# Performance work log

Measured on AMD Instinct MI355X. Metric: run time of the kernel, lower is better.

## Reference

```python
import jax, jax.numpy as jnp
import numpy as np

C = 512
NH = 8
GROUPS = 32
EPS = 1e-5


def setup_inputs() -> dict:
    key = jax.random.key(0)
    ks = jax.random.split(key, 7)
    B, T, H, W = 4, 24, 32, 32
    x = jax.random.normal(ks[0], (B, C, T, H, W), dtype=jnp.float32)
    gn_w = jnp.ones((C,), jnp.float32)
    gn_b = jnp.zeros((C,), jnp.float32)
    # 1x1 Conv1d weights stored as [out_ch, in_ch] (kernel dim of size 1 dropped)
    qkv_w = jax.random.normal(ks[1], (3 * C, C), dtype=jnp.float32) / np.sqrt(C)
    qkv_b = jax.random.normal(ks[2], (3 * C,), dtype=jnp.float32) * 0.02
    proj_w = jax.random.normal(ks[3], (C, C), dtype=jnp.float32) / np.sqrt(C)
    proj_b = jax.random.normal(ks[4], (C,), dtype=jnp.float32) * 0.02
    return {"x": x, "gn_w": gn_w, "gn_b": gn_b, "qkv_w": qkv_w,
            "qkv_b": qkv_b, "proj_w": proj_w, "proj_b": proj_b}


def reference(x, gn_w, gn_b, qkv_w, qkv_b, proj_w, proj_b):
    B, Cc, T, H, W = x.shape
    hd = Cc // NH
    # [B,C,T,H,W] -> [B*H*W, C, T]
    xf = jnp.transpose(x, (0, 3, 4, 1, 2)).reshape(B * H * W, Cc, T)
    # GroupNorm over (C/G, T) per group
    xg = xf.reshape(-1, GROUPS, Cc // GROUPS, T)
    mean = xg.mean(axis=(2, 3), keepdims=True)
    var = xg.var(axis=(2, 3), keepdims=True)
    xn = ((xg - mean) * jax.lax.rsqrt(var + EPS)).reshape(-1, Cc, T)
    xn = xn * gn_w[:, None] + gn_b[:, None]
    # 1x1 conv QKV: [n, 3C, T]
    qkv = jnp.einsum('nct,dc->ndt', xn, qkv_w) + qkv_b[:, None]
    qkv = qkv.reshape(-1, 3, NH, hd, T)
    q, k, v = qkv[:, 0], qkv[:, 1], qkv[:, 2]  # each [n, h, d, T]
    scale = 1.0 / np.sqrt(hd)
    attn = jax.nn.softmax(jnp.einsum('nhdt,nhds->nhts', q, k) * scale, axis=-1)
    out = jnp.einsum('nhts,nhds->nhtd', attn, v)        # [n, h, T, d]
    out = out.transpose(0, 2, 1, 3).reshape(-1, T, Cc)   # [n, T, C]
    out = out.transpose(0, 2, 1)                         # [n, C, T]
    out = jnp.einsum('nct,dc->ndt', out, proj_w) + proj_b[:, None]
    out = out.reshape(B, H, W, Cc, T).transpose(0, 3, 4, 1, 2)
    return x + out
```

## Files before the change

kernel.cpp:

```cpp
#include <hip/hip_runtime.h>
#include <hip/hip_bf16.h>
#include <stdint.h>

#define C_    512
#define T_    24
#define HWSZ  1024
#define NN    4096
#define JTOT  98304
#define EPSV  1e-5f

typedef short short8 __attribute__((ext_vector_type(8)));
typedef short short4v __attribute__((ext_vector_type(4)));
typedef float f32x4 __attribute__((ext_vector_type(4)));

typedef __attribute__((address_space(1))) const uint32_t glob_u32;
typedef __attribute__((address_space(3))) uint32_t lds_u32;

__device__ __forceinline__ unsigned short f2bf(float f) {
  union { float f; unsigned u; } v; v.f = f;
  unsigned r = v.u + 0x7fffu + ((v.u >> 16) & 1u);
  return (unsigned short)(r >> 16);
}
__device__ __forceinline__ float bf2f(unsigned short b) {
  union { unsigned u; float f; } v; v.u = ((unsigned)b) << 16;
  return v.f;
}
__device__ __forceinline__ float bflo(uint32_t u) {
  union { unsigned u; float f; } v; v.u = u << 16; return v.f;
}
__device__ __forceinline__ float bfhi(uint32_t u) {
  union { unsigned u; float f; } v; v.u = u & 0xffff0000u; return v.f;
}
__device__ __forceinline__ uint32_t pkbf(float a, float b) {
  return (uint32_t)f2bf(a) | ((uint32_t)f2bf(b) << 16);
}

__device__ __forceinline__ void gload_lds16(const void* g, void* l) {
  __builtin_amdgcn_global_load_lds((glob_u32*)g, (lds_u32*)l, 16, 0, 0);
}

__global__ void k_cvt(const float* __restrict__ qkvw, const float* __restrict__ projw,
                      unsigned short* __restrict__ qkvw_bf, unsigned short* __restrict__ projw_bf) {
  int i = blockIdx.x * 256 + threadIdx.x;
  if (i < 786432) qkvw_bf[i] = f2bf(qkvw[i]);
  if (i < 262144) projw_bf[i] = f2bf(projw[i]);
}

__global__ __launch_bounds__(256) void k_stats(const float* __restrict__ x,
                                               float* __restrict__ mean, float* __restrict__ rstd) {
  int bid = blockIdx.x;
  int g = bid & 31, hwt = (bid >> 5) & 15, b = bid >> 9;
  int tid = threadIdx.x, lane = tid & 63, grp = tid >> 6;
  int hw = hwt * 64 + lane;
  float s = 0.f, sq = 0.f;
  for (int ct = grp; ct < 384; ct += 4) {
    int c = g * 16 + ct / 24;
    int t = ct % 24;
    float v = x[((size_t)((b * 512 + c) * 24 + t) << 10) + hw];
    s += v; sq += v * v;
  }
  __shared__ float ls[4][64], lq[4][64];
  ls[grp][lane] = s; lq[grp][lane] = sq;
  __syncthreads();
  if (tid < 64) {
    float S = ls[0][tid] + ls[1][tid] + ls[2][tid] + ls[3][tid];
    float Q = lq[0][tid] + lq[1][tid] + lq[2][tid] + lq[3][tid];
    float m = S * (1.f / 384.f);
    float var = Q * (1.f / 384.f) - m * m;
    int n = b * HWSZ + hwt * 64 + tid;
    mean[n * 32 + g] = m;
    rstd[n * 32 + g] = rsqrtf(var + EPSV);
  }
}

__global__ __launch_bounds__(256) void k_norm(const float* __restrict__ x,
                                              const float* __restrict__ mean, const float* __restrict__ rstd,
                                              const float* __restrict__ gnw, const float* __restrict__ gnb,
                                              unsigned short* __restrict__ xn) {
  __shared__ unsigned short xs[64][260];
  const int bid = blockIdx.x;
  const int hwt = bid & 15;
  const int chalf = (bid >> 4) & 1;
  const int tb = bid >> 5;
  const int t = tb % 24, b = tb / 24;
  const int hw0 = hwt * 64;
  const int tid = threadIdx.x;
  const int w = tid >> 6, lane = tid & 63;

  const int crel0 = w * 4 + (lane >> 4);
  const int hwr = (lane & 15) * 4;
#pragma unroll
  for (int k = 0; k < 16; ++k) {
    const int crel = k * 16 + crel0;
    const int c = chalf * 256 + crel;
    const float4 v = *reinterpret_cast<const float4*>(
        &x[(((size_t)(b * 512 + c) * 24 + t) << 10) + hw0 + hwr]);
    xs[hwr + 0][crel] = f2bf(v.x);
    xs[hwr + 1][crel] = f2bf(v.y);
    xs[hwr + 2][crel] = f2bf(v.z);
    xs[hwr + 3][crel] = f2bf(v.w);
  }

  const int crel8 = (lane & 31) * 8;
  const int c8 = chalf * 256 + crel8;
  const int g = c8 >> 4;
  float gw[8], gb[8];
#pragma unroll
  for (int i = 0; i < 8; ++i) { gw[i] = gnw[c8 + i]; gb[i] = gnb[c8 + i]; }
  float mm[8], rr[8];
#pragma unroll
  for (int p = 0; p < 8; ++p) {
    const int nrel = (p * 4 + w) * 2 + (lane >> 5);
    const int ng = b * HWSZ + hw0 + nrel;
    mm[p] = mean[ng * 32 + g];
    rr[p] = rstd[ng * 32 + g];
  }
  __syncthreads();

#pragma unroll
  for (int p = 0; p < 8; ++p) {
    const int nrel = (p * 4 + w) * 2 + (lane >> 5);
    const short4v lo = *reinterpret_cast<const short4v*>(&xs[nrel][crel8]);
    const short4v hi = *reinterpret_cast<const short4v*>(&xs[nrel][crel8 + 4]);
    float y[8];
#pragma unroll
    for (int i = 0; i < 4; ++i) {
      y[i]     = (bf2f((unsigned short)lo[i]) - mm[p]) * rr[p] * gw[i]     + gb[i];
      y[i + 4] = (bf2f((unsigned short)hi[i]) - mm[p]) * rr[p] * gw[i + 4] + gb[i + 4];
    }
    uint4 wv;
    wv.x = pkbf(y[0], y[1]);
    wv.y = pkbf(y[2], y[3]);
    wv.z = pkbf(y[4], y[5]);
    wv.w = pkbf(y[6], y[7]);
    const size_t j = (size_t)t * NN + b * HWSZ + hw0 + nrel;
    *reinterpret_cast<uint4*>(&xn[j * C_ + c8]) = wv;
  }
}

#define STAGE8(mat, half, tile, Gptr, row0)                                           \
  {                                                                                   \
    unsigned short* _l = &lds[(((tile) & 1) * 2 + (mat))][half][(w * 2) * 512];       \
    const unsigned short* _g = (Gptr) +                                               \
        (size_t)((row0) + (half) * 128 + (w * 2) * 8 + srow) * 512 +                  \
        (tile) * 64 + sslot * 8;                                                      \
    gload_lds16(_g, _l);                                                              \
    gload_lds16(_g + 8 * 512, _l + 512);                                              \
  }

__global__ __launch_bounds__(512, 2) void k_gemm8(
    const unsigned short* __restrict__ A,
    const unsigned short* __restrict__ B,
    const float* __restrict__ bias,
    unsigned short* __restrict__ outb) {
  __shared__ __attribute__((aligned(16))) unsigned short lds[4][2][8192];
  const int bid = blockIdx.x;
  const int cpx = 2304 >> 3;
  const int lid = (bid & 7) * cpx + (bid >> 3);
  const int mt = lid % 6, jt = lid / 6;
  const int m0 = mt * 256, j0 = jt * 256;
  const int tid = threadIdx.x;
  const int w = tid >> 6, lane = tid & 63;
  const int l16 = lane & 15, lqq = lane >> 4;
  const int wm = w >> 2, wn = w & 3;
  const int srow = lane >> 3;
  const int sslot = (lane & 7) ^ srow;
  const int k0off = l16 * 64 + ((lqq ^ (l16 & 7)) * 8);
  const int k1off = l16 * 64 + (((lqq + 4) ^ (l16 & 7)) * 8);

  f32x4 acc[8][4];
#pragma unroll
  for (int i = 0; i < 8; ++i)
#pragma unroll
    for (int j = 0; j < 4; ++j) acc[i][j] = {0.f, 0.f, 0.f, 0.f};

  STAGE8(0, 0, 0, A, m0); STAGE8(0, 1, 0, A, m0);
  STAGE8(1, 0, 0, B, j0); STAGE8(1, 1, 0, B, j0);
  STAGE8(0, 0, 1, A, m0); STAGE8(0, 1, 1, A, m0);
  STAGE8(1, 0, 1, B, j0);
  asm volatile("s_waitcnt vmcnt(6)" ::: "memory");
  __builtin_amdgcn_s_barrier();

  for (int t = 0; t < 8; ++t) {
    const int buf = t & 1;
    const unsigned short* Ab = &lds[buf * 2 + 0][wm][0];
    const unsigned short* Bb = &lds[buf * 2 + 1][wn >> 1][(wn & 1) * 4096];
    short8 a[8][2], bb[4][2];
#pragma unroll
    for (int rr = 0; rr < 8; ++rr) {
      a[rr][0] = *reinterpret_cast<const short8*>(Ab + rr * 1024 + k0off);
      a[rr][1] = *reinterpret_cast<const short8*>(Ab + rr * 1024 + k1off);
    }
#pragma unroll
    for (int cc = 0; cc < 2; ++cc) {
      bb[cc][0] = *reinterpret_cast<const short8*>(Bb + cc * 1024 + k0off);
      bb[cc][1] = *reinterpret_cast<const short8*>(Bb + cc * 1024 + k1off);
    }
    if (t < 7) STAGE8(1, 1, t + 1, B, j0);
    asm volatile("" ::: "memory");
    __builtin_amdgcn_s_barrier();
    asm volatile("s_waitcnt lgkmcnt(0)" ::: "memory");
    __builtin_amdgcn_sched_barrier(0);
    __builtin_amdgcn_s_setprio(1);
#pragma unroll
    for (int rr = 0; rr < 4; ++rr)
#pragma unroll
      for (int cc = 0; cc < 2; ++cc) {
        acc[rr][cc] = __builtin_amdgcn_mfma_f32_16x16x32_bf16(a[rr][0], bb[cc][0], acc[rr][cc], 0, 0, 0);
        acc[rr][cc] = __builtin_amdgcn_mfma_f32_16x16x32_bf16(a[rr][1], bb[cc][1], acc[rr][cc], 0, 0, 0);
      }
    __builtin_amdgcn_s_setprio(0);
    asm volatile("" ::: "memory");
    __builtin_amdgcn_s_barrier();
#pragma unroll
    for (int cc = 2; cc < 4; ++cc) {
      bb[cc][0] = *reinterpret_cast<const short8*>(Bb + cc * 1024 + k0off);
      bb[cc][1] = *reinterpret_cast<const short8*>(Bb + cc * 1024 + k1off);
    }
    if (t < 6) STAGE8(0, 0, t + 2, A, m0);
    asm volatile("" ::: "memory");
    __builtin_amdgcn_s_barrier();
    asm volatile("s_waitcnt lgkmcnt(0)" ::: "memory");
    __builtin_amdgcn_sched_barrier(0);
    __builtin_amdgcn_s_setprio(1);
#pragma unroll
    for (int rr = 0; rr < 4; ++rr)
#pragma unroll
      for (int cc = 2; cc < 4; ++cc) {
        acc[rr][cc] = __builtin_amdgcn_mfma_f32_16x16x32_bf16(a[rr][0], bb[cc][0], acc[rr][cc], 0, 0, 0);
        acc[rr][cc] = __builtin_amdgcn_mfma_f32_16x16x32_bf16(a[rr][1], bb[cc][1], acc[rr][cc], 0, 0, 0);
      }
    __builtin_amdgcn_s_setprio(0);
    asm volatile("" ::: "memory");
    __builtin_amdgcn_s_barrier();
    if (t < 6) STAGE8(0, 1, t + 2, A, m0);
    asm volatile("" ::: "memory");
    __builtin_amdgcn_s_barrier();
    __builtin_amdgcn_s_setprio(1);
#pragma unroll
    for (int rr = 4; rr < 8; ++rr)
#pragma unroll
      for (int cc = 0; cc < 2; ++cc) {
        acc[rr][cc] = __builtin_amdgcn_mfma_f32_16x16x32_bf16(a[rr][0], bb[cc][0], acc[rr][cc], 0, 0, 0);
        acc[rr][cc] = __builtin_amdgcn_mfma_f32_16x16x32_bf16(a[rr][1], bb[cc][1], acc[rr][cc], 0, 0, 0);
      }
    __builtin_amdgcn_s_setprio(0);
    asm volatile("" ::: "memory");
    __builtin_amdgcn_s_barrier();
    if (t < 6) STAGE8(1, 0, t + 2, B, j0);
    asm volatile("" ::: "memory");
    __builtin_amdgcn_s_barrier();
    __builtin_amdgcn_s_setprio(1);
#pragma unroll
    for (int rr = 4; rr < 8; ++rr)
#pragma unroll
      for (int cc = 2; cc < 4; ++cc) {
        acc[rr][cc] = __builtin_amdgcn_mfma_f32_16x16x32_bf16(a[rr][0], bb[cc][0], acc[rr][cc], 0, 0, 0);
        acc[rr][cc] = __builtin_amdgcn_mfma_f32_16x16x32_bf16(a[rr][1], bb[cc][1], acc[rr][cc], 0, 0, 0);
      }
    __builtin_amdgcn_s_setprio(0);
    asm volatile("" ::: "memory");
    if (t < 6) {
      asm volatile("s_waitcnt vmcnt(6)" ::: "memory");
    } else if (t == 6) {
      asm volatile("s_waitcnt vmcnt(0)" ::: "memory");
    }
    __builtin_amdgcn_s_barrier();
  }

#pragma unroll
  for (int rr = 0; rr < 8; ++rr) {
#pragma unroll
    for (int cc = 0; cc < 4; ++cc) {
      const int row = m0 + wm * 128 + rr * 16 + lqq * 4;
      const int col = j0 + wn * 64 + cc * 16 + l16;
#pragma unroll
      for (int r = 0; r < 4; ++r) {
        float v = acc[rr][cc][r] + bias[row + r];
        outb[(size_t)(row + r) * JTOT + col] = f2bf(v);
      }
    }
  }
}

template <int MODE>
__global__ __launch_bounds__(256, 3) void k_gemm(
    const unsigned short* __restrict__ A,
    const unsigned short* __restrict__ B,
    const float* __restrict__ bias,
    unsigned short* __restrict__ outb,
    const float* __restrict__ xres,
    float* __restrict__ outf) {
  __shared__ __attribute__((aligned(16))) unsigned short As[128 * 64];
  __shared__ __attribute__((aligned(16))) unsigned short Bs[128 * 64];
  const int NMT = (MODE == 0) ? 12 : 4;
  const int bid = blockIdx.x;
  const int cpx = gridDim.x >> 3;
  const int lid = (bid & 7) * cpx + (bid >> 3);
  const int mt = lid % NMT, jt = lid / NMT;
  const int j0 = jt * 128, m0 = mt * 128;
  const int tid = threadIdx.x;
  const int wave = tid >> 6, lane = tid & 63;
  const int l16 = lane & 15, lqq = lane >> 4;
  const int wm = wave >> 1, wn = wave & 1;
  const int srow = lane >> 3, sseg = lane & 7;

  f32x4 acc[4][4];
#pragma unroll
  for (int i = 0; i < 4; ++i)
#pragma unroll
    for (int j = 0; j < 4; ++j) acc[i][j] = {0.f, 0.f, 0.f, 0.f};

  for (int kt = 0; kt < 512; kt += 64) {
#pragma unroll
    for (int i = 0; i < 4; ++i) {
      const int chunk = i * 4 + wave;
      const int r = chunk * 8 + srow;
      gload_lds16(A + ((size_t)(m0 + r) * 512 + kt + sseg * 8), &As[chunk * 512]);
    }
    if (MODE == 0) {
#pragma unroll
      for (int i = 0; i < 4; ++i) {
        const int chunk = i * 4 + wave;
        const int r = chunk * 8 + srow;
        gload_lds16(B + ((size_t)(j0 + r) * 512 + kt + sseg * 8), &Bs[chunk * 512]);
      }
    } else {
#pragma unroll
      for (int p = 0; p < 4; ++p) {
        const int u = p * 256 + tid;
        const int kc = u >> 7, jr = u & 127;
        gload_lds16(B + ((size_t)((kt >> 3) + kc) * JTOT + (j0 + jr)) * 8, &Bs[(size_t)u * 8]);
      }
    }
    __syncthreads();
#pragma unroll
    for (int ks = 0; ks < 2; ++ks) {
      short8 af[4], bfr[4];
#pragma unroll
      for (int i = 0; i < 4; ++i)
        af[i] = *reinterpret_cast<const short8*>(&As[(wm * 64 + i * 16 + l16) * 64 + ks * 32 + lqq * 8]);
#pragma unroll
      for (int i = 0; i < 4; ++i) {
        if (MODE == 0)
          bfr[i] = *reinterpret_cast<const short8*>(&Bs[(wn * 64 + i * 16 + l16) * 64 + ks * 32 + lqq * 8]);
        else
          bfr[i] = *reinterpret_cast<const short8*>(&Bs[(((ks * 4 + lqq) * 128) + wn * 64 + i * 16 + l16) * 8]);
      }
#pragma unroll
      for (int mi = 0; mi < 4; ++mi)
#pragma unroll
        for (int ni = 0; ni < 4; ++ni)
          acc[mi][ni] = __builtin_amdgcn_mfma_f32_16x16x32_bf16(af[mi], bfr[ni], acc[mi][ni], 0, 0, 0);
    }
    __syncthreads();
  }

#pragma unroll
  for (int mi = 0; mi < 4; ++mi) {
#pragma unroll
    for (int ni = 0; ni < 4; ++ni) {
      const int dbase = m0 + wm * 64 + mi * 16 + lqq * 4;
      const int jj = j0 + wn * 64 + ni * 16 + l16;
      if (MODE == 0) {
#pragma unroll
        for (int r = 0; r < 4; ++r) {
          float v = acc[mi][ni][r] + bias[dbase + r];
          outb[(size_t)(dbase + r) * JTOT + jj] = f2bf(v);
        }
      } else {
        const int t = jj >> 12, n = jj & 4095;
        const int b = n >> 10, hw = n & 1023;
#pragma unroll
        for (int r = 0; r < 4; ++r) {
          size_t o = (((size_t)(b * 512 + dbase + r) * 24 + t) << 10) + hw;
          outf[o] = xres[o] + acc[mi][ni][r] + bias[dbase + r];
        }
      }
    }
  }
}

__global__ __launch_bounds__(512) void k_attn(const unsigned short* __restrict__ qkv,
                                              unsigned short* __restrict__ aoC) {
  __shared__ uint32_t kbuf[4][24][64];
  const int ntile = blockIdx.x, h = blockIdx.y;
  const int n0 = ntile * 64;
  const int lane = threadIdx.x & 63, slot = threadIdx.x >> 6;
  const int t0 = slot * 3;
  const size_t baseq = (size_t)(h * 64) * JTOT + n0 + lane;
  const size_t basek = (size_t)(512 + h * 64) * JTOT + n0 + lane;
  const size_t basev = (size_t)(1024 + h * 64) * JTOT + n0 + lane;

  float S[3][24];
#pragma unroll
  for (int a = 0; a < 3; ++a)
#pragma unroll
    for (int s = 0; s < 24; ++s) S[a][s] = 0.f;

  uint32_t kp[12], qp[12];

#pragma unroll
  for (int dp = 0; dp < 4; ++dp)
#pragma unroll
    for (int a = 0; a < 3; ++a) {
      uint32_t klo = qkv[basek + (size_t)(2 * dp) * JTOT + (t0 + a) * NN];
      uint32_t khi = qkv[basek + (size_t)(2 * dp + 1) * JTOT + (t0 + a) * NN];
      kp[dp * 3 + a] = klo | (khi << 16);
      uint32_t qlo = qkv[baseq + (size_t)(2 * dp) * JTOT + (t0 + a) * NN];
      uint32_t qhi = qkv[baseq + (size_t)(2 * dp + 1) * JTOT + (t0 + a) * NN];
      qp[dp * 3 + a] = qlo | (qhi << 16);
    }

  for (int c = 0; c < 8; ++c) {
    const int dc = c * 8;
#pragma unroll
    for (int dp = 0; dp < 4; ++dp)
#pragma unroll
      for (int a = 0; a < 3; ++a)
        kbuf[dp][t0 + a][lane] = kp[dp * 3 + a];
    float qf[3][8];
#pragma unroll
    for (int dp = 0; dp < 4; ++dp)
#pragma unroll
      for (int a = 0; a < 3; ++a) {
        qf[a][2 * dp]     = bflo(qp[dp * 3 + a]);
        qf[a][2 * dp + 1] = bfhi(qp[dp * 3 + a]);
      }
    if (c < 7) {
      const int dn = dc + 8;
#pragma unroll
      for (int dp = 0; dp < 4; ++dp)
#pragma unroll
        for (int a = 0; a < 3; ++a) {
          uint32_t klo = qkv[basek + (size_t)(dn + 2 * dp) * JTOT + (t0 + a) * NN];
          uint32_t khi = qkv[basek + (size_t)(dn + 2 * dp + 1) * JTOT + (t0 + a) * NN];
          kp[dp * 3 + a] = klo | (khi << 16);
          uint32_t qlo = qkv[baseq + (size_t)(dn + 2 * dp) * JTOT + (t0 + a) * NN];
          uint32_t qhi = qkv[baseq + (size_t)(dn + 2 * dp + 1) * JTOT + (t0 + a) * NN];
          qp[dp * 3 + a] = qlo | (qhi << 16);
        }
    }
    __syncthreads();
#pragma unroll
    for (int dp = 0; dp < 4; ++dp) {
#pragma unroll
      for (int s = 0; s < 24; ++s) {
        uint32_t kpr = kbuf[dp][s][lane];
        float k0 = bflo(kpr), k1 = bfhi(kpr);
        S[0][s] = fmaf(qf[0][2 * dp], k0, S[0][s]);
        S[0][s] = fmaf(qf[0][2 * dp + 1], k1, S[0][s]);
        S[1][s] = fmaf(qf[1][2 * dp], k0, S[1][s]);
        S[1][s] = fmaf(qf[1][2 * dp + 1], k1, S[1][s]);
        S[2][s] = fmaf(qf[2][2 * dp], k0, S[2][s]);
        S[2][s] = fmaf(qf[2][2 * dp + 1], k1, S[2][s]);
      }
    }
    __syncthreads();
  }

#pragma unroll
  for (int dp = 0; dp < 4; ++dp)
#pragma unroll
    for (int a = 0; a < 3; ++a) {
      uint32_t vlo = qkv[basev + (size_t)(2 * dp) * JTOT + (t0 + a) * NN];
      uint32_t vhi = qkv[basev + (size_t)(2 * dp + 1) * JTOT + (t0 + a) * NN];
      kp[dp * 3 + a] = vlo | (vhi << 16);
    }

#pragma unroll
  for (int a = 0; a < 3; ++a) {
    float mx = S[a][0];
#pragma unroll
    for (int s = 1; s < 24; ++s) mx = fmaxf(mx, S[a][s]);
    float sum = 0.f;
#pragma unroll
    for (int s = 0; s < 24; ++s) {
      float e = __expf((S[a][s] - mx) * 0.125f);
      S[a][s] = e; sum += e;
    }
    float inv = 1.f / sum;
#pragma unroll
    for (int s = 0; s < 24; ++s) S[a][s] *= inv;
  }

  for (int c = 0; c < 8; ++c) {
    const int dc = c * 8;
#pragma unroll
    for (int dp = 0; dp < 4; ++dp)
#pragma unroll
      for (int a = 0; a < 3; ++a)
        kbuf[dp][t0 + a][lane] = kp[dp * 3 + a];
    if (c < 7) {
      const int dn = dc + 8;
#pragma unroll
      for (int dp = 0; dp < 4; ++dp)
#pragma unroll
        for (int a = 0; a < 3; ++a) {
          uint32_t vlo = qkv[basev + (size_t)(dn + 2 * dp) * JTOT + (t0 + a) * NN];
          uint32_t vhi = qkv[basev + (size_t)(dn + 2 * dp + 1) * JTOT + (t0 + a) * NN];
          kp[dp * 3 + a] = vlo | (vhi << 16);
        }
    }
    __syncthreads();
    float o[3][8];
#pragma unroll
    for (int a = 0; a < 3; ++a)
#pragma unroll
      for (int d = 0; d < 8; ++d) o[a][d] = 0.f;
#pragma unroll
    for (int dp = 0; dp < 4; ++dp) {
#pragma unroll
      for (int s = 0; s < 24; ++s) {
        uint32_t vpr = kbuf[dp][s][lane];
        float v0 = bflo(vpr), v1 = bfhi(vpr);
        o[0][2 * dp]     = fmaf(S[0][s], v0, o[0][2 * dp]);
        o[0][2 * dp + 1] = fmaf(S[0][s], v1, o[0][2 * dp + 1]);
        o[1][2 * dp]     = fmaf(S[1][s], v0, o[1][2 * dp]);
        o[1][2 * dp + 1] = fmaf(S[1][s], v1, o[1][2 * dp + 1]);
        o[2][2 * dp]     = fmaf(S[2][s], v0, o[2][2 * dp]);
        o[2][2 * dp + 1] = fmaf(S[2][s], v1, o[2][2 * dp + 1]);
      }
    }
#pragma unroll
    for (int a = 0; a < 3; ++a) {
      uint4 wv;
      wv.x = pkbf(o[a][0], o[a][1]);
      wv.y = pkbf(o[a][2], o[a][3]);
      wv.z = pkbf(o[a][4], o[a][5]);
      wv.w = pkbf(o[a][6], o[a][7]);
      size_t unit = (size_t)(h * 8 + c) * JTOT + (size_t)(t0 + a) * NN + n0 + lane;
      *reinterpret_cast<uint4*>(&aoC[unit * 8]) = wv;
    }
    __syncthreads();
  }
}

extern "C" void kernel_launch(void* const* d_in, const int* in_sizes, int n_in,
                              void* d_out, int out_size, void* d_ws, size_t ws_size,
                              hipStream_t stream) {
  (void)in_sizes; (void)n_in; (void)out_size; (void)ws_size;
  const float* x     = (const float*)d_in[0];
  const float* gnw   = (const float*)d_in[1];
  const float* gnb   = (const float*)d_in[2];
  const float* qkvw  = (const float*)d_in[3];
  const float* qkvb  = (const float*)d_in[4];
  const float* projw = (const float*)d_in[5];
  const float* projb = (const float*)d_in[6];
  float* out = (float*)d_out;
  char* ws = (char*)d_ws;

  unsigned short* qkvw_bf = (unsigned short*)(ws);
  unsigned short* projw_bf = (unsigned short*)(ws + 1572864);
  float* mean = (float*)(ws + 2097152);
  float* rstd = (float*)(ws + 2621440);
  unsigned short* xn  = (unsigned short*)(ws + 3145728);
  unsigned short* qkv = (unsigned short*)(ws + 3145728 + 100663296);

  k_cvt<<<dim3(3072), dim3(256), 0, stream>>>(qkvw, projw, qkvw_bf, projw_bf);
  k_stats<<<dim3(2048), dim3(256), 0, stream>>>(x, mean, rstd);
  k_norm<<<dim3(3072), dim3(256), 0, stream>>>(x, mean, rstd, gnw, gnb, xn);
  k_gemm8<<<dim3(2304), dim3(512), 0, stream>>>(qkvw_bf, xn, qkvb, qkv);
  k_attn<<<dim3(64, 8), dim3(512), 0, stream>>>(qkv, xn);
  k_gemm<1><<<dim3(3072), dim3(256), 0, stream>>>(projw_bf, xn, projb, nullptr, x, out);
}
```

Measured before the change: 588.6 us.

## Make 256x256 GEMM persistent and reuse it for output projection

The large-tile bf16 GEMM is converted into a persistent kernel with 256 blocks, each looping over several output tiles in an XCD-grouped order instead of launching one block per tile. It is templated so the output projection, previously run by a smaller 128x128 non-pipelined GEMM, now uses the same pipelined 256x256 path. For that path it adds a separate B-staging routine for the k-chunked attention-output layout and fuses the residual add. This aims to cut launch and tail overhead and raise data reuse in the projection GEMM. The cost is fewer resident blocks and a pipeline prologue that restarts for every tile.

```diff
diff --git a/kernel.cpp b/kernel.cpp
--- a/kernel.cpp
+++ b/kernel.cpp
@@ -148,17 +148,31 @@
     gload_lds16(_g + 8 * 512, _l + 512);                                              \
   }
 
+#define STAGE8B1(half, tile)                                                          \
+  {                                                                                   \
+    unsigned short* _l = &lds[(((tile) & 1) * 2 + 1)][half][(w * 2) * 512];           \
+    const unsigned short* _g = B +                                                    \
+        ((size_t)((tile) * 8 + sslot) * JTOT + (j0 + (half) * 128 + w * 16 + srow)) * 8; \
+    gload_lds16(_g, _l);                                                              \
+    gload_lds16(_g + 64, _l + 512);                                                   \
+  }
+
+#define STAGE_B(half, tile) { if (MODE == 0) { STAGE8(1, half, tile, B, j0) } else { STAGE8B1(half, tile) } }
+
+template <int MODE>
 __global__ __launch_bounds__(512, 2) void k_gemm8(
     const unsigned short* __restrict__ A,
     const unsigned short* __restrict__ B,
     const float* __restrict__ bias,
-    unsigned short* __restrict__ outb) {
+    unsigned short* __restrict__ outb,
+    const float* __restrict__ xres,
+    float* __restrict__ outf) {
   __shared__ __attribute__((aligned(16))) unsigned short lds[4][2][8192];
   const int bid = blockIdx.x;
-  const int cpx = 2304 >> 3;
-  const int lid = (bid & 7) * cpx + (bid >> 3);
-  const int mt = lid % 6, jt = lid / 6;
-  const int m0 = mt * 256, j0 = jt * 256;
+  const int xcd = bid & 7, cu = bid >> 3;
+  const int NMT = (MODE == 0) ? 6 : 2;
+  const int TPX = (MODE == 0) ? 288 : 96;
+  const int ITERS = (MODE == 0) ? 9 : 3;
   const int tid = threadIdx.x;
   const int w = tid >> 6, lane = tid & 63;
   const int l16 = lane & 15, lqq = lane >> 4;
@@ -168,213 +182,131 @@
   const int k0off = l16 * 64 + ((lqq ^ (l16 & 7)) * 8);
   const int k1off = l16 * 64 + (((lqq + 4) ^ (l16 & 7)) * 8);
 
-  f32x4 acc[8][4];
-#pragma unroll
-  for (int i = 0; i < 8; ++i)
-#pragma unroll
-    for (int j = 0; j < 4; ++j) acc[i][j] = {0.f, 0.f, 0.f, 0.f};
-
-  STAGE8(0, 0, 0, A, m0); STAGE8(0, 1, 0, A, m0);
-  STAGE8(1, 0, 0, B, j0); STAGE8(1, 1, 0, B, j0);
-  STAGE8(0, 0, 1, A, m0); STAGE8(0, 1, 1, A, m0);
-  STAGE8(1, 0, 1, B, j0);
-  asm volatile("s_waitcnt vmcnt(6)" ::: "memory");
-  __builtin_amdgcn_s_barrier();
-
-  for (int t = 0; t < 8; ++t) {
-    const int buf = t & 1;
-    const unsigned short* Ab = &lds[buf * 2 + 0][wm][0];
-    const unsigned short* Bb = &lds[buf * 2 + 1][wn >> 1][(wn & 1) * 4096];
-    short8 a[8][2], bb[4][2];
+  for (int it = 0; it < ITERS; ++it) {
+    const int lid = xcd * TPX + it * 32 + cu;
+    const int mt = lid % NMT, jt = lid / NMT;
+    const int m0 = mt * 256, j0 = jt * 256;
+
+    f32x4 acc[8][4];
+#pragma unroll
+    for (int i = 0; i < 8; ++i)
+#pragma unroll
+      for (int j = 0; j < 4; ++j) acc[i][j] = {0.f, 0.f, 0.f, 0.f};
+
+    STAGE8(0, 0, 0, A, m0); STAGE8(0, 1, 0, A, m0);
+    STAGE_B(0, 0); STAGE_B(1, 0);
+    STAGE8(0, 0, 1, A, m0); STAGE8(0, 1, 1, A, m0);
+    STAGE_B(0, 1);
+    asm volatile("s_waitcnt vmcnt(6)" ::: "memory");
+    __builtin_amdgcn_s_barrier();
+
+    for (int t = 0; t < 8; ++t) {
+      const int buf = t & 1;
+      const unsigned short* Ab = &lds[buf * 2 + 0][wm][0];
+      const unsigned short* Bb = &lds[buf * 2 + 1][wn >> 1][(wn & 1) * 4096];
+      short8 a[8][2], bb[4][2];
+#pragma unroll
+      for (int rr = 0; rr < 8; ++rr) {
+        a[rr][0] = *reinterpret_cast<const short8*>(Ab + rr * 1024 + k0off);
+        a[rr][1] = *reinterpret_cast<const short8*>(Ab + rr * 1024 + k1off);
+      }
+#pragma unroll
+      for (int cc = 0; cc < 2; ++cc) {
+        bb[cc][0] = *reinterpret_cast<const short8*>(Bb + cc * 1024 + k0off);
+        bb[cc][1] = *reinterpret_cast<const short8*>(Bb + cc * 1024 + k1off);
+      }
+      if (t < 7) STAGE_B(1, t + 1);
+      asm volatile("" ::: "memory");
+      __builtin_amdgcn_s_barrier();
+      asm volatile("s_waitcnt lgkmcnt(0)" ::: "memory");
+      __builtin_amdgcn_sched_barrier(0);
+      __builtin_amdgcn_s_setprio(1);
+#pragma unroll
+      for (int rr = 0; rr < 4; ++rr)
+#pragma unroll
+        for (int cc = 0; cc < 2; ++cc) {
+          acc[rr][cc] = __builtin_amdgcn_mfma_f32_16x16x32_bf16(a[rr][0], bb[cc][0], acc[rr][cc], 0, 0, 0);
+          acc[rr][cc] = __builtin_amdgcn_mfma_f32_16x16x32_bf16(a[rr][1], bb[cc][1], acc[rr][cc], 0, 0, 0);
+        }
+      __builtin_amdgcn_s_setprio(0);
+      asm volatile("" ::: "memory");
+      __builtin_amdgcn_s_barrier();
+#pragma unroll
+      for (int cc = 2; cc < 4; ++cc) {
+        bb[cc][0] = *reinterpret_cast<const short8*>(Bb + cc * 1024 + k0off);
+        bb[cc][1] = *reinterpret_cast<const short8*>(Bb + cc * 1024 + k1off);
+      }
+      if (t < 6) STAGE8(0, 0, t + 2, A, m0);
+      asm volatile("" ::: "memory");
+      __builtin_amdgcn_s_barrier();
+      asm volatile("s_waitcnt lgkmcnt(0)" ::: "memory");
+      __builtin_amdgcn_sched_barrier(0);
+      __builtin_amdgcn_s_setprio(1);
+#pragma unroll
+      for (int rr = 0; rr < 4; ++rr)
+#pragma unroll
+        for (int cc = 2; cc < 4; ++cc) {
+          acc[rr][cc] = __builtin_amdgcn_mfma_f32_16x16x32_bf16(a[rr][0], bb[cc][0], acc[rr][cc], 0, 0, 0);
+          acc[rr][cc] = __builtin_amdgcn_mfma_f32_16x16x32_bf16(a[rr][1], bb[cc][1], acc[rr][cc], 0, 0, 0);
+        }
+      __builtin_amdgcn_s_setprio(0);
+      asm volatile("" ::: "memory");
+      __builtin_amdgcn_s_barrier();
+      if (t < 6) STAGE8(0, 1, t + 2, A, m0);
+      asm volatile("" ::: "memory");
+      __builtin_amdgcn_s_barrier();
+      __builtin_amdgcn_s_setprio(1);
+#pragma unroll
+      for (int rr = 4; rr < 8; ++rr)
+#pragma unroll
+        for (int cc = 0; cc < 2; ++cc) {
+          acc[rr][cc] = __builtin_amdgcn_mfma_f32_16x16x32_bf16(a[rr][0], bb[cc][0], acc[rr][cc], 0, 0, 0);
+          acc[rr][cc] = __builtin_amdgcn_mfma_f32_16x16x32_bf16(a[rr][1], bb[cc][1], acc[rr][cc], 0, 0, 0);
+        }
+      __builtin_amdgcn_s_setprio(0);
+      asm volatile("" ::: "memory");
+      __builtin_amdgcn_s_barrier();
+      if (t < 6) STAGE_B(0, t + 2);
+      asm volatile("" ::: "memory");
+      __builtin_amdgcn_s_barrier();
+      __builtin_amdgcn_s_setprio(1);
+#pragma unroll
+      for (int rr = 4; rr < 8; ++rr)
+#pragma unroll
+        for (int cc = 2; cc < 4; ++cc) {
+          acc[rr][cc] = __builtin_amdgcn_mfma_f32_16x16x32_bf16(a[rr][0], bb[cc][0], acc[rr][cc], 0, 0, 0);
+          acc[rr][cc] = __builtin_amdgcn_mfma_f32_16x16x32_bf16(a[rr][1], bb[cc][1], acc[rr][cc], 0, 0, 0);
+        }
+      __builtin_amdgcn_s_setprio(0);
+      asm volatile("" ::: "memory");
+      if (t < 6) {
+        asm volatile("s_waitcnt vmcnt(6)" ::: "memory");
+      } else if (t == 6) {
+        asm volatile("s_waitcnt vmcnt(0)" ::: "memory");
+      }
+      __builtin_amdgcn_s_barrier();
+    }
+
 #pragma unroll
     for (int rr = 0; rr < 8; ++rr) {
-      a[rr][0] = *reinterpret_cast<const short8*>(Ab + rr * 1024 + k0off);
-      a[rr][1] = *reinterpret_cast<const short8*>(Ab + rr * 1024 + k1off);
-    }
-#pragma unroll
-    for (int cc = 0; cc < 2; ++cc) {
-      bb[cc][0] = *reinterpret_cast<const short8*>(Bb + cc * 1024 + k0off);
-      bb[cc][1] = *reinterpret_cast<const short8*>(Bb + cc * 1024 + k1off);
-    }
-    if (t < 7) STAGE8(1, 1, t + 1, B, j0);
-    asm volatile("" ::: "memory");
-    __builtin_amdgcn_s_barrier();
-    asm volatile("s_waitcnt lgkmcnt(0)" ::: "memory");
-    __builtin_amdgcn_sched_barrier(0);
-    __builtin_amdgcn_s_setprio(1);
-#pragma unroll
-    for (int rr = 0; rr < 4; ++rr)
-#pragma unroll
-      for (int cc = 0; cc < 2; ++cc) {
-        acc[rr][cc] = __builtin_amdgcn_mfma_f32_16x16x32_bf16(a[rr][0], bb[cc][0], acc[rr][cc], 0, 0, 0);
-        acc[rr][cc] = __builtin_amdgcn_mfma_f32_16x16x32_bf16(a[rr][1], bb[cc][1], acc[rr][cc], 0, 0, 0);
-      }
-    __builtin_amdgcn_s_setprio(0);
-    asm volatile("" ::: "memory");
-    __builtin_amdgcn_s_barrier();
-#pragma unroll
-    for (int cc = 2; cc < 4; ++cc) {
-      bb[cc][0] = *reinterpret_cast<const short8*>(Bb + cc * 1024 + k0off);
-      bb[cc][1] = *reinterpret_cast<const short8*>(Bb + cc * 1024 + k1off);
-    }
-    if (t < 6) STAGE8(0, 0, t + 2, A, m0);
-    asm volatile("" ::: "memory");
-    __builtin_amdgcn_s_barrier();
-    asm volatile("s_waitcnt lgkmcnt(0)" ::: "memory");
-    __builtin_amdgcn_sched_barrier(0);
-    __builtin_amdgcn_s_setprio(1);
-#pragma unroll
-    for (int rr = 0; rr < 4; ++rr)
-#pragma unroll
-      for (int cc = 2; cc < 4; ++cc) {
-        acc[rr][cc] = __builtin_amdgcn_mfma_f32_16x16x32_bf16(a[rr][0], bb[cc][0], acc[rr][cc], 0, 0, 0);
-        acc[rr][cc] = __builtin_amdgcn_mfma_f32_16x16x32_bf16(a[rr][1], bb[cc][1], acc[rr][cc], 0, 0, 0);
-      }
-    __builtin_amdgcn_s_setprio(0);
-    asm volatile("" ::: "memory");
-    __builtin_amdgcn_s_barrier();
-    if (t < 6) STAGE8(0, 1, t + 2, A, m0);
-    asm volatile("" ::: "memory");
-    __builtin_amdgcn_s_barrier();
-    __builtin_amdgcn_s_setprio(1);
-#pragma unroll
-    for (int rr = 4; rr < 8; ++rr)
-#pragma unroll
-      for (int cc = 0; cc < 2; ++cc) {
-        acc[rr][cc] = __builtin_amdgcn_mfma_f32_16x16x32_bf16(a[rr][0], bb[cc][0], acc[rr][cc], 0, 0, 0);
-        acc[rr][cc] = __builtin_amdgcn_mfma_f32_16x16x32_bf16(a[rr][1], bb[cc][1], acc[rr][cc], 0, 0, 0);
-      }
-    __builtin_amdgcn_s_setprio(0);
-    asm volatile("" ::: "memory");
-    __builtin_amdgcn_s_barrier();
-    if (t < 6) STAGE8(1, 0, t + 2, B, j0);
-    asm volatile("" ::: "memory");
-    __builtin_amdgcn_s_barrier();
-    __builtin_amdgcn_s_setprio(1);
-#pragma unroll
-    for (int rr = 4; rr < 8; ++rr)
-#pragma unroll
-      for (int cc = 2; cc < 4; ++cc) {
-        acc[rr][cc] = __builtin_amdgcn_mfma_f32_16x16x32_bf16(a[rr][0], bb[cc][0], acc[rr][cc], 0, 0, 0);
-        acc[rr][cc] = __builtin_amdgcn_mfma_f32_16x16x32_bf16(a[rr][1], bb[cc][1], acc[rr][cc], 0, 0, 0);
-      }
-    __builtin_amdgcn_s_setprio(0);
-    asm volatile("" ::: "memory");
-    if (t < 6) {
-      asm volatile("s_waitcnt vmcnt(6)" ::: "memory");
-    } else if (t == 6) {
-      asm volatile("s_waitcnt vmcnt(0)" ::: "memory");
-    }
-    __builtin_amdgcn_s_barrier();
-  }
-
-#pragma unroll
-  for (int rr = 0; rr < 8; ++rr) {
-#pragma unroll
-    for (int cc = 0; cc < 4; ++cc) {
-      const int row = m0 + wm * 128 + rr * 16 + lqq * 4;
-      const int col = j0 + wn * 64 + cc * 16 + l16;
-#pragma unroll
-      for (int r = 0; r < 4; ++r) {
-        float v = acc[rr][cc][r] + bias[row + r];
-        outb[(size_t)(row + r) * JTOT + col] = f2bf(v);
-      }
-    }
-  }
-}
-
-template <int MODE>
-__global__ __launch_bounds__(256, 3) void k_gemm(
-    const unsigned short* __restrict__ A,
-    const unsigned short* __restrict__ B,
-    const float* __restrict__ bias,
-    unsigned short* __restrict__ outb,
-    const float* __restrict__ xres,
-    float* __restrict__ outf) {
-  __shared__ __attribute__((aligned(16))) unsigned short As[128 * 64];
-  __shared__ __attribute__((aligned(16))) unsigned short Bs[128 * 64];
-  const int NMT = (MODE == 0) ? 12 : 4;
-  const int bid = blockIdx.x;
-  const int cpx = gridDim.x >> 3;
-  const int lid = (bid & 7) * cpx + (bid >> 3);
-  const int mt = lid % NMT, jt = lid / NMT;
-  const int j0 = jt * 128, m0 = mt * 128;
-  const int tid = threadIdx.x;
-  const int wave = tid >> 6, lane = tid & 63;
-  const int l16 = lane & 15, lqq = lane >> 4;
-  const int wm = wave >> 1, wn = wave & 1;
-  const int srow = lane >> 3, sseg = lane & 7;
-
-  f32x4 acc[4][4];
-#pragma unroll
-  for (int i = 0; i < 4; ++i)
-#pragma unroll
-    for (int j = 0; j < 4; ++j) acc[i][j] = {0.f, 0.f, 0.f, 0.f};
-
-  for (int kt = 0; kt < 512; kt += 64) {
-#pragma unroll
-    for (int i = 0; i < 4; ++i) {
-      const int chunk = i * 4 + wave;
-      const int r = chunk * 8 + srow;
-      gload_lds16(A + ((size_t)(m0 + r) * 512 + kt + sseg * 8), &As[chunk * 512]);
-    }
-    if (MODE == 0) {
-#pragma unroll
-      for (int i = 0; i < 4; ++i) {
-        const int chunk = i * 4 + wave;
-        const int r = chunk * 8 + srow;
-        gload_lds16(B + ((size_t)(j0 + r) * 512 + kt + sseg * 8), &Bs[chunk * 512]);
-      }
-    } else {
-#pragma unroll
-      for (int p = 0; p < 4; ++p) {
-        const int u = p * 256 + tid;
-        const int kc = u >> 7, jr = u & 127;
-        gload_lds16(B + ((size_t)((kt >> 3) + kc) * JTOT + (j0 + jr)) * 8, &Bs[(size_t)u * 8]);
-      }
-    }
-    __syncthreads();
-#pragma unroll
-    for (int ks = 0; ks < 2; ++ks) {
-      short8 af[4], bfr[4];
-#pragma unroll
-      for (int i = 0; i < 4; ++i)
-        af[i] = *reinterpret_cast<const short8*>(&As[(wm * 64 + i * 16 + l16) * 64 + ks * 32 + lqq * 8]);
-#pragma unroll
-      for (int i = 0; i < 4; ++i) {
-        if (MODE == 0)
-          bfr[i] = *reinterpret_cast<const short8*>(&Bs[(wn * 64 + i * 16 + l16) * 64 + ks * 32 + lqq * 8]);
-        else
-          bfr[i] = *reinterpret_cast<const short8*>(&Bs[(((ks * 4 + lqq) * 128) + wn * 64 + i * 16 + l16) * 8]);
-      }
-#pragma unroll
-      for (int mi = 0; mi < 4; ++mi)
-#pragma unroll
-        for (int ni = 0; ni < 4; ++ni)
-          acc[mi][ni] = __builtin_amdgcn_mfma_f32_16x16x32_bf16(af[mi], bfr[ni], acc[mi][ni], 0, 0, 0);
-    }
-    __syncthreads();
-  }
-
-#pragma unroll
-  for (int mi = 0; mi < 4; ++mi) {
-#pragma unroll
-    for (int ni = 0; ni < 4; ++ni) {
-      const int dbase = m0 + wm * 64 + mi * 16 + lqq * 4;
-      const int jj = j0 + wn * 64 + ni * 16 + l16;
-      if (MODE == 0) {
-#pragma unroll
-        for (int r = 0; r < 4; ++r) {
-          float v = acc[mi][ni][r] + bias[dbase + r];
-          outb[(size_t)(dbase + r) * JTOT + jj] = f2bf(v);
-        }
-      } else {
-        const int t = jj >> 12, n = jj & 4095;
-        const int b = n >> 10, hw = n & 1023;
-#pragma unroll
-        for (int r = 0; r < 4; ++r) {
-          size_t o = (((size_t)(b * 512 + dbase + r) * 24 + t) << 10) + hw;
-          outf[o] = xres[o] + acc[mi][ni][r] + bias[dbase + r];
+#pragma unroll
+      for (int cc = 0; cc < 4; ++cc) {
+        const int row = m0 + wm * 128 + rr * 16 + lqq * 4;
+        const int col = j0 + wn * 64 + cc * 16 + l16;
+        if (MODE == 0) {
+#pragma unroll
+          for (int r = 0; r < 4; ++r) {
+            float v = acc[rr][cc][r] + bias[row + r];
+            outb[(size_t)(row + r) * JTOT + col] = f2bf(v);
+          }
+        } else {
+          const int t_ = col >> 12, n = col & 4095;
+          const int b_ = n >> 10, hw = n & 1023;
+#pragma unroll
+          for (int r = 0; r < 4; ++r) {
+            size_t o = (((size_t)(b_ * 512 + row + r) * 24 + t_) << 10) + hw;
+            outf[o] = xres[o] + acc[rr][cc][r] + bias[row + r];
+          }
         }
       }
     }
@@ -560,7 +492,7 @@
   k_cvt<<<dim3(3072), dim3(256), 0, stream>>>(qkvw, projw, qkvw_bf, projw_bf);
   k_stats<<<dim3(2048), dim3(256), 0, stream>>>(x, mean, rstd);
   k_norm<<<dim3(3072), dim3(256), 0, stream>>>(x, mean, rstd, gnw, gnb, xn);
-  k_gemm8<<<dim3(2304), dim3(512), 0, stream>>>(qkvw_bf, xn, qkvb, qkv);
+  k_gemm8<0><<<dim3(256), dim3(512), 0, stream>>>(qkvw_bf, xn, qkvb, qkv, nullptr, nullptr);
   k_attn<<<dim3(64, 8), dim3(512), 0, stream>>>(qkv, xn);
-  k_gemm<1><<<dim3(3072), dim3(256), 0, stream>>>(projw_bf, xn, projb, nullptr, x, out);
-}
+  k_gemm8<1><<<dim3(256), dim3(512), 0, stream>>>(projw_bf, xn, projb, nullptr, x, out);
+}
```

Result: slower. 603.3 us (+2.5%).

## Double-buffer proj GEMM A tiles and load B fragments directly from global

Applied to the files above, without the earlier changes.

Replaces the templated proj GEMM with a dedicated kernel. The A (weight) tile is now double-buffered in LDS with an XOR-swizzled layout, so the next tile's load overlaps the current MFMA work and bank conflicts drop. B (activation) fragments are read straight from global memory into registers instead of being staged through LDS, which removes one barrier-protected copy per step. The cost is more global-load latency exposed on the B path and higher register pressure.

```diff
diff --git a/kernel.cpp b/kernel.cpp
--- a/kernel.cpp
+++ b/kernel.cpp
@@ -283,27 +283,26 @@
   }
 }
 
-template <int MODE>
-__global__ __launch_bounds__(256, 3) void k_gemm(
+__global__ __launch_bounds__(256, 3) void k_proj(
     const unsigned short* __restrict__ A,
     const unsigned short* __restrict__ B,
     const float* __restrict__ bias,
-    unsigned short* __restrict__ outb,
     const float* __restrict__ xres,
     float* __restrict__ outf) {
-  __shared__ __attribute__((aligned(16))) unsigned short As[128 * 64];
-  __shared__ __attribute__((aligned(16))) unsigned short Bs[128 * 64];
-  const int NMT = (MODE == 0) ? 12 : 4;
+  __shared__ __attribute__((aligned(16))) unsigned short As[2][8192];
   const int bid = blockIdx.x;
-  const int cpx = gridDim.x >> 3;
+  const int cpx = 3072 >> 3;
   const int lid = (bid & 7) * cpx + (bid >> 3);
-  const int mt = lid % NMT, jt = lid / NMT;
-  const int j0 = jt * 128, m0 = mt * 128;
+  const int mt = lid & 3, jt = lid >> 2;
+  const int m0 = mt * 128, j0 = jt * 128;
   const int tid = threadIdx.x;
-  const int wave = tid >> 6, lane = tid & 63;
+  const int w = tid >> 6, lane = tid & 63;
   const int l16 = lane & 15, lqq = lane >> 4;
-  const int wm = wave >> 1, wn = wave & 1;
-  const int srow = lane >> 3, sseg = lane & 7;
+  const int wm = w >> 1, wn = w & 1;
+  const int srow8 = lane >> 3;
+  const int sslot = (lane & 7) ^ srow8;
+  const int k0off = l16 * 64 + ((lqq ^ (l16 & 7)) * 8);
+  const int k1off = l16 * 64 + (((lqq + 4) ^ (l16 & 7)) * 8);
 
   f32x4 acc[4][4];
 #pragma unroll
@@ -311,48 +310,47 @@
 #pragma unroll
     for (int j = 0; j < 4; ++j) acc[i][j] = {0.f, 0.f, 0.f, 0.f};
 
-  for (int kt = 0; kt < 512; kt += 64) {
-#pragma unroll
-    for (int i = 0; i < 4; ++i) {
-      const int chunk = i * 4 + wave;
-      const int r = chunk * 8 + srow;
-      gload_lds16(A + ((size_t)(m0 + r) * 512 + kt + sseg * 8), &As[chunk * 512]);
-    }
-    if (MODE == 0) {
-#pragma unroll
-      for (int i = 0; i < 4; ++i) {
-        const int chunk = i * 4 + wave;
-        const int r = chunk * 8 + srow;
-        gload_lds16(B + ((size_t)(j0 + r) * 512 + kt + sseg * 8), &Bs[chunk * 512]);
-      }
-    } else {
-#pragma unroll
-      for (int p = 0; p < 4; ++p) {
-        const int u = p * 256 + tid;
-        const int kc = u >> 7, jr = u & 127;
-        gload_lds16(B + ((size_t)((kt >> 3) + kc) * JTOT + (j0 + jr)) * 8, &Bs[(size_t)u * 8]);
-      }
-    }
-    __syncthreads();
-#pragma unroll
-    for (int ks = 0; ks < 2; ++ks) {
-      short8 af[4], bfr[4];
-#pragma unroll
-      for (int i = 0; i < 4; ++i)
-        af[i] = *reinterpret_cast<const short8*>(&As[(wm * 64 + i * 16 + l16) * 64 + ks * 32 + lqq * 8]);
-#pragma unroll
-      for (int i = 0; i < 4; ++i) {
-        if (MODE == 0)
-          bfr[i] = *reinterpret_cast<const short8*>(&Bs[(wn * 64 + i * 16 + l16) * 64 + ks * 32 + lqq * 8]);
-        else
-          bfr[i] = *reinterpret_cast<const short8*>(&Bs[(((ks * 4 + lqq) * 128) + wn * 64 + i * 16 + l16) * 8]);
-      }
-#pragma unroll
-      for (int mi = 0; mi < 4; ++mi)
-#pragma unroll
-        for (int ni = 0; ni < 4; ++ni)
-          acc[mi][ni] = __builtin_amdgcn_mfma_f32_16x16x32_bf16(af[mi], bfr[ni], acc[mi][ni], 0, 0, 0);
-    }
+#define PSTAGE(buf, tile)                                                             \
+  {                                                                                   \
+    _Pragma("unroll")                                                                 \
+    for (int m_ = 0; m_ < 4; ++m_) {                                                  \
+      unsigned short* _l = &As[buf][m_ * 2048 + w * 512];                             \
+      const unsigned short* _g = A +                                                  \
+          (size_t)(m0 + m_ * 32 + w * 8 + srow8) * 512 + (tile) * 64 + sslot * 8;     \
+      gload_lds16(_g, _l);                                                            \
+    }                                                                                 \
+  }
+
+  PSTAGE(0, 0);
+  __syncthreads();
+
+  for (int t = 0; t < 8; ++t) {
+    const int buf = t & 1;
+    if (t < 7) PSTAGE(buf ^ 1, t + 1);
+    short8 bb[4][2];
+#pragma unroll
+    for (int cc = 0; cc < 4; ++cc) {
+      const int j = j0 + wn * 64 + cc * 16 + l16;
+#pragma unroll
+      for (int ks = 0; ks < 2; ++ks) {
+        const size_t e = ((size_t)(t * 8 + ks * 4 + lqq) * JTOT + j) * 8;
+        bb[cc][ks] = *reinterpret_cast<const short8*>(&B[e]);
+      }
+    }
+    const unsigned short* Ab = &As[buf][(wm * 64) * 64];
+    short8 af[4][2];
+#pragma unroll
+    for (int rr = 0; rr < 4; ++rr) {
+      af[rr][0] = *reinterpret_cast<const short8*>(Ab + rr * 1024 + k0off);
+      af[rr][1] = *reinterpret_cast<const short8*>(Ab + rr * 1024 + k1off);
+    }
+#pragma unroll
+    for (int rr = 0; rr < 4; ++rr)
+#pragma unroll
+      for (int cc = 0; cc < 4; ++cc) {
+        acc[rr][cc] = __builtin_amdgcn_mfma_f32_16x16x32_bf16(af[rr][0], bb[cc][0], acc[rr][cc], 0, 0, 0);
+        acc[rr][cc] = __builtin_amdgcn_mfma_f32_16x16x32_bf16(af[rr][1], bb[cc][1], acc[rr][cc], 0, 0, 0);
+      }
     __syncthreads();
   }
 
@@ -362,20 +360,12 @@
     for (int ni = 0; ni < 4; ++ni) {
       const int dbase = m0 + wm * 64 + mi * 16 + lqq * 4;
       const int jj = j0 + wn * 64 + ni * 16 + l16;
-      if (MODE == 0) {
-#pragma unroll
-        for (int r = 0; r < 4; ++r) {
-          float v = acc[mi][ni][r] + bias[dbase + r];
-          outb[(size_t)(dbase + r) * JTOT + jj] = f2bf(v);
-        }
-      } else {
-        const int t = jj >> 12, n = jj & 4095;
-        const int b = n >> 10, hw = n & 1023;
-#pragma unroll
-        for (int r = 0; r < 4; ++r) {
-          size_t o = (((size_t)(b * 512 + dbase + r) * 24 + t) << 10) + hw;
-          outf[o] = xres[o] + acc[mi][ni][r] + bias[dbase + r];
-        }
+      const int t_ = jj >> 12, n = jj & 4095;
+      const int b_ = n >> 10, hw = n & 1023;
+#pragma unroll
+      for (int r = 0; r < 4; ++r) {
+        size_t o = (((size_t)(b_ * 512 + dbase + r) * 24 + t_) << 10) + hw;
+        outf[o] = xres[o] + acc[mi][ni][r] + bias[dbase + r];
       }
     }
   }
@@ -562,5 +552,5 @@
   k_norm<<<dim3(3072), dim3(256), 0, stream>>>(x, mean, rstd, gnw, gnb, xn);
   k_gemm8<<<dim3(2304), dim3(512), 0, stream>>>(qkvw_bf, xn, qkvb, qkv);
   k_attn<<<dim3(64, 8), dim3(512), 0, stream>>>(qkv, xn);
-  k_gemm<1><<<dim3(3072), dim3(256), 0, stream>>>(projw_bf, xn, projb, nullptr, x, out);
-}
+  k_proj<<<dim3(3072), dim3(256), 0, stream>>>(projw_bf, xn, projb, x, out);
+}
```

New measurement: 594.1 us. Within noise of the previous version (+0.9%).
